# Optimization experiments

Measured on AMD Instinct MI355X. Metric: run time of the kernel, lower is better.

Reference implementation:

```python
import jax, jax.numpy as jnp
import numpy as np

N, F, D = 32, 1024, 512
H = 2 * D  # dim * ratio
EPS = 1e-5


def batchnorm1d(x, gamma, beta):
    # x: (N, F, L); BatchNorm1d over channel dim F, stats over (N, L) (training mode, biased var)
    mean = jnp.mean(x, axis=(0, 2), keepdims=True)
    var = jnp.var(x, axis=(0, 2), keepdims=True)
    xn = (x - mean) * jax.lax.rsqrt(var + EPS)
    return xn * gamma[None, :, None] + beta[None, :, None]


def setup_inputs() -> dict:
    key = jax.random.key(0)
    ks = jax.random.split(key, 5)
    x = jax.random.normal(ks[0], (N, F, D), dtype=jnp.float32)
    W0 = jax.random.normal(ks[1], (H, D), dtype=jnp.float32) * 0.02  # Linear(D->H) weight (out,in)
    b0 = jnp.zeros((H,), jnp.float32)
    W1 = jax.random.normal(ks[2], (D, H), dtype=jnp.float32) * 0.02  # Linear(H->D)
    b1 = jnp.zeros((D,), jnp.float32)
    Wc = jax.random.normal(ks[3], (F, F), dtype=jnp.float32) * 0.02  # Conv1d k=1 weight (out_ch,in_ch)
    bc = jnp.zeros((F,), jnp.float32)
    ones = jnp.ones((F,), jnp.float32)
    zeros = jnp.zeros((F,), jnp.float32)
    return {
        "x": x,
        "W0": W0, "b0": b0, "g0": ones, "be0": zeros,
        "W1": W1, "b1": b1, "g1": ones, "be1": zeros,
        "gf": ones, "bf": zeros,
        "Wc": Wc, "bc": bc,
        "go": ones, "bo": zeros,
    }


def reference(x, W0, b0, g0, be0, W1, b1, g1, be1, gf, bf, Wc, bc, go, bo):
    # proj_mlp0: Linear(D->H) + BN1d(F)
    v = jnp.einsum('nfd,hd->nfh', x, W0) + b0  # (N, F, H)
    v = batchnorm1d(v, g0, be0)
    # correlation: bmm(v, v^T) -> softsign -> bmm(w, v)
    w = jnp.einsum('nfh,ngh->nfg', v, v)  # (N, F, F)
    w = w / (1.0 + jnp.abs(w))  # softsign
    v = jnp.einsum('nfg,ngh->nfh', w, v)  # (N, F, H)
    # proj_mlp1: Linear(H->D) + BN1d(F)
    v = jnp.einsum('nfh,dh->nfd', v, W1) + b1  # (N, F, D)
    v = batchnorm1d(v, g1, be1)
    # feed_norm(v + x)
    xr = batchnorm1d(v + x, gf, bf)
    # proj_conv: Conv1d(F->F, kernel=1) over channel dim
    v = jnp.einsum('oi,nid->nod', Wc, xr) + bc[None, :, None]
    return batchnorm1d(v + xr, go, bo)
```

## Files before the change

### kernel.cpp

```cpp
#include <hip/hip_runtime.h>
#include <stdint.h>

#define NB 32
#define FC 1024
#define DD 512
#define HH 1024
#define BN_EPS 1e-5f

typedef unsigned short u16;
typedef unsigned int u32;
typedef __attribute__((ext_vector_type(8))) short bf16x8;
typedef __attribute__((ext_vector_type(4))) float f32x4;
typedef __attribute__((ext_vector_type(8))) unsigned short ushort8v;

#define AS1 __attribute__((address_space(1)))
#define AS3 __attribute__((address_space(3)))

__device__ __forceinline__ float b2f(u16 u) {
    union { u32 i; float f; } v;
    v.i = ((u32)u) << 16;
    return v.f;
}
__device__ __forceinline__ u16 f2b(float f) {
    union { float f; u32 i; } v;
    v.f = f;
    const u32 b = v.i;
    return (u16)((b + 0x7FFFu + ((b >> 16) & 1u)) >> 16);
}

__device__ __forceinline__ void gld16(const u16* g, u16* l) {
    __builtin_amdgcn_global_load_lds((const AS1 u32*)g, (AS3 u32*)l, 16, 0, 0);
}

__device__ __forceinline__ void swizzle_tiles(int& mt, int& nt, int& zt) {
    const int gx = gridDim.x, gy = gridDim.y, gz = gridDim.z;
    const int mzTot = gy * gz;
    if ((mzTot & 7) != 0) { nt = blockIdx.x; mt = blockIdx.y; zt = blockIdx.z; return; }
    long lin = ((long)blockIdx.z * gy + blockIdx.y) * gx + blockIdx.x;
    const int slab = mzTot >> 3;
    const int xcd = (int)(lin & 7);
    const long idx = lin >> 3;
    nt = (int)(idx % gx);
    const int mz = (int)(idx / gx) + xcd * slab;
    mt = mz % gy;
    zt = mz / gy;
}

__global__ __launch_bounds__(256) void detect_dtype(
    const u32* __restrict__ x, int* __restrict__ flag)
{
    __shared__ int cnt[256];
    int c = 0;
    for (int i = threadIdx.x; i < 4096; i += 256) {
        const u32 lo = x[i] & 0xFFFFu;
        const u32 e = (lo >> 7) & 0xFFu;
        if (e >= 0x68u && e <= 0x85u) c++;
    }
    cnt[threadIdx.x] = c;
    __syncthreads();
    for (int s = 128; s > 0; s >>= 1) {
        if (threadIdx.x < (unsigned)s) cnt[threadIdx.x] += cnt[threadIdx.x + s];
        __syncthreads();
    }
    if (threadIdx.x == 0) flag[0] = (cnt[0] > 2048) ? 1 : 0;
}

__global__ __launch_bounds__(256) void zero_partials(float* __restrict__ sp) {
    sp[blockIdx.x * 256 + threadIdx.x] = 0.0f;
}

__global__ __launch_bounds__(256) void fold_bn(
    const float* __restrict__ sp, const u16* __restrict__ gamma,
    const u16* __restrict__ beta, float* __restrict__ ssf, float invCnt)
{
    const int f = blockIdx.x * 256 + threadIdx.x;
    if (f < FC) {
        const float mean = sp[f] * invCnt;
        const float var  = sp[FC + f] * invCnt - mean * mean;
        const float rstd = rsqrtf(var + BN_EPS);
        const float sc   = b2f(gamma[f]) * rstd;
        ssf[f]      = sc;
        ssf[FC + f] = b2f(beta[f]) - mean * sc;
    }
}

__global__ __launch_bounds__(256) void convert_to_bf16(
    const void* __restrict__ src, u16* __restrict__ dst, long n4,
    const int* __restrict__ flag)
{
    const bool isbf = (*flag != 0);
    long i4 = (long)blockIdx.x * blockDim.x + threadIdx.x;
    const long stride = (long)gridDim.x * blockDim.x;
    for (; i4 < n4; i4 += stride) {
        const long i = i4 << 2;
        if (isbf) {
            *(ushort4*)(dst + i) = *(const ushort4*)((const u16*)src + i);
        } else {
            const float4 v = *(const float4*)((const float*)src + i);
            ushort4 o;
            o.x = f2b(v.x); o.y = f2b(v.y); o.z = f2b(v.z); o.w = f2b(v.w);
            *(ushort4*)(dst + i) = o;
        }
    }
}

struct ConvArgs { const void* src[14]; long off[14]; long n4[14]; };
__global__ __launch_bounds__(256) void convert_params(
    ConvArgs a, u16* __restrict__ dst, const int* __restrict__ flag)
{
    const bool isbf = (*flag != 0);
    const long stride = (long)gridDim.x * blockDim.x;
    for (int s = 0; s < 14; ++s) {
        const long n4 = a.n4[s];
        u16* d = dst + a.off[s];
        const void* sp = a.src[s];
        for (long i4 = (long)blockIdx.x * blockDim.x + threadIdx.x; i4 < n4;
             i4 += stride) {
            const long i = i4 << 2;
            if (isbf) {
                *(ushort4*)(d + i) = *(const ushort4*)((const u16*)sp + i);
            } else {
                const float4 v = *(const float4*)((const float*)sp + i);
                ushort4 o;
                o.x = f2b(v.x); o.y = f2b(v.y); o.z = f2b(v.z); o.w = f2b(v.w);
                *(ushort4*)(d + i) = o;
            }
        }
    }
}

template<bool BIAS, bool SOFTSIGN, bool STATS, bool RESID>
__global__ __launch_bounds__(512, 4) void gemm128x256_nt(
    const u16* __restrict__ A, const u16* __restrict__ B,
    const u16* __restrict__ bias, const u16* __restrict__ resid,
    u16* __restrict__ C, float* __restrict__ sp, int sym,
    int M, int N, int K, int lda, int ldb, int ldc,
    long sA, long sB, long sC)
{
    extern __shared__ char smem[];

    int mt, nt, zt;
    swizzle_tiles(mt, nt, zt);
    if (sym && mt < 2 * nt) return;
    const u16* Ab = A + (long)zt * sA + (long)(mt * 128) * lda;
    const u16* Bb = B + (long)zt * sB + (long)(nt * 256) * ldb;
    C += (long)zt * sC;
    const u16* RP = RESID ? (resid + (long)zt * sC) : nullptr;

    const int tid  = threadIdx.x;
    const int lane = tid & 63;
    const int wv   = tid >> 6;
    const int wrr  = (wv >> 2) * 64;
    const int wc   = (wv & 3) * 64;
    const int lm   = lane & 15;
    const int q    = lane >> 4;

    int aOff[4], bOff[4];
    #pragma unroll
    for (int i = 0; i < 4; ++i) {
        const int r = wrr + i * 16 + lm;
        aOff[i] = r * 64 + ((q ^ ((r >> 1) & 3)) << 4);
    }
    #pragma unroll
    for (int j = 0; j < 4; ++j) {
        const int r = wc + j * 16 + lm;
        bOff[j] = r * 64 + ((q ^ ((r >> 1) & 3)) << 4);
    }

    const int rw = lane >> 2, qs = lane & 3;
    const int rA  = wv * 16 + rw;
    const int rB0 = wv * 32 + rw;
    const int rB1 = wv * 32 + 16 + rw;
    const u16* pA  = Ab + (long)rA  * lda + ((qs ^ ((rA  >> 1) & 3)) << 3);
    const u16* pB0 = Bb + (long)rB0 * ldb + ((qs ^ ((rB0 >> 1) & 3)) << 3);
    const u16* pB1 = Bb + (long)rB1 * ldb + ((qs ^ ((rB1 >> 1) & 3)) << 3);
    const int ldsA  = wv * 1024;
    const int ldsB0 = wv * 2048;
    const int ldsB1 = wv * 2048 + 1024;

#define STAGE(bufOff, kofs) { \
    gld16(pA  + (kofs), (u16*)(smem + (bufOff) + ldsA)); \
    gld16(pB0 + (kofs), (u16*)(smem + (bufOff) + 8192 + ldsB0)); \
    gld16(pB1 + (kofs), (u16*)(smem + (bufOff) + 8192 + ldsB1)); }

#define RINGBAR() { \
    asm volatile("s_waitcnt vmcnt(3) lgkmcnt(0)" ::: "memory"); \
    __builtin_amdgcn_sched_barrier(0); \
    __builtin_amdgcn_s_barrier(); \
    __builtin_amdgcn_sched_barrier(0); }

    f32x4 acc[4][4] = {};

    const int NT = K >> 5;

    STAGE(0, 0);
    STAGE(24576, 32);
    RINGBAR();

    int cur = 0, nxt = 2;
    for (int t = 0; t < NT; ++t) {
        const int bo = cur * 24576;
        const int bn = nxt * 24576;
        const int kn = (((t + 2) < NT) ? (t + 2) : (NT - 1)) * 32;
        STAGE(bn, kn);

        bf16x8 a[4], b[4];
        const char* baseA = smem + bo;
        const char* baseB = smem + bo + 8192;
        #pragma unroll
        for (int i = 0; i < 4; ++i) a[i] = *(const bf16x8*)(baseA + aOff[i]);
        #pragma unroll
        for (int j = 0; j < 4; ++j) b[j] = *(const bf16x8*)(baseB + bOff[j]);

        #pragma unroll
        for (int i = 0; i < 4; ++i)
            #pragma unroll
            for (int j = 0; j < 4; ++j)
                acc[i][j] = __builtin_amdgcn_mfma_f32_16x16x32_bf16(
                    a[i], b[j], acc[i][j], 0, 0, 0);

        RINGBAR();
        cur = (cur == 2) ? 0 : cur + 1;
        nxt = (nxt == 2) ? 0 : nxt + 1;
    }

#undef STAGE
#undef RINGBAR

    asm volatile("s_waitcnt vmcnt(0)" ::: "memory");
    __builtin_amdgcn_sched_barrier(0);
    __syncthreads();

    float* rep = (float*)smem + wv * (16 * 65);
    const int rr = lane >> 2;
    const int cg = lane & 3;
    const int m0 = mt * 128;
    const int n0 = nt * 256;
    #pragma unroll
    for (int i = 0; i < 4; ++i) {
        #pragma unroll
        for (int j = 0; j < 4; ++j) {
            const int col = 16 * j + lm;
            const float bj = BIAS ? b2f(bias[n0 + wc + col]) : 0.0f;
            #pragma unroll
            for (int r = 0; r < 4; ++r) {
                float v = acc[i][j][r] + bj;
                if (SOFTSIGN) v = v / (1.0f + fabsf(v));
                rep[(q * 4 + r) * 65 + col] = v;
            }
        }
        const int row = m0 + wrr + 16 * i + rr;
        const float* lr = rep + rr * 65 + cg * 16;
        float4 f0 = *(const float4*)(lr + 0);
        float4 f1 = *(const float4*)(lr + 4);
        float4 f2 = *(const float4*)(lr + 8);
        float4 f3 = *(const float4*)(lr + 12);
        if (RESID) {
            const u16* rp = RP + (long)row * ldc + n0 + wc + cg * 16;
            const ushort8v ra = *(const ushort8v*)rp;
            const ushort8v rb = *(const ushort8v*)(rp + 8);
            f0.x += b2f(ra[0]); f0.y += b2f(ra[1]); f0.z += b2f(ra[2]); f0.w += b2f(ra[3]);
            f1.x += b2f(ra[4]); f1.y += b2f(ra[5]); f1.z += b2f(ra[6]); f1.w += b2f(ra[7]);
            f2.x += b2f(rb[0]); f2.y += b2f(rb[1]); f2.z += b2f(rb[2]); f2.w += b2f(rb[3]);
            f3.x += b2f(rb[4]); f3.y += b2f(rb[5]); f3.z += b2f(rb[6]); f3.w += b2f(rb[7]);
        }
        if (STATS) {
            float s1 = (f0.x + f0.y + f0.z + f0.w) + (f1.x + f1.y + f1.z + f1.w)
                     + (f2.x + f2.y + f2.z + f2.w) + (f3.x + f3.y + f3.z + f3.w);
            float s2 = f0.x*f0.x + f0.y*f0.y + f0.z*f0.z + f0.w*f0.w
                     + f1.x*f1.x + f1.y*f1.y + f1.z*f1.z + f1.w*f1.w
                     + f2.x*f2.x + f2.y*f2.y + f2.z*f2.z + f2.w*f2.w
                     + f3.x*f3.x + f3.y*f3.y + f3.z*f3.z + f3.w*f3.w;
            s1 += __shfl_xor(s1, 1); s1 += __shfl_xor(s1, 2);
            s2 += __shfl_xor(s2, 1); s2 += __shfl_xor(s2, 2);
            if (cg == 0) {
                const int ch = row & (FC - 1);
                atomicAdd(&sp[ch], s1);
                atomicAdd(&sp[FC + ch], s2);
            }
        }
        ushort8v o0, o1;
        o0[0] = f2b(f0.x); o0[1] = f2b(f0.y); o0[2] = f2b(f0.z); o0[3] = f2b(f0.w);
        o0[4] = f2b(f1.x); o0[5] = f2b(f1.y); o0[6] = f2b(f1.z); o0[7] = f2b(f1.w);
        o1[0] = f2b(f2.x); o1[1] = f2b(f2.y); o1[2] = f2b(f2.z); o1[3] = f2b(f2.w);
        o1[4] = f2b(f3.x); o1[5] = f2b(f3.y); o1[6] = f2b(f3.z); o1[7] = f2b(f3.w);
        u16* cp = C + (long)row * ldc + n0 + wc + cg * 16;
        *(ushort8v*)cp = o0;
        *(ushort8v*)(cp + 8) = o1;
    }
}

__global__ __launch_bounds__(256) void mirror_upper(
    u16* __restrict__ W, long sW)
{
    const int MTt[12] = {0,1, 0,1,2,3, 0,1,2,3,4,5};
    const int NTt[12] = {1,1, 2,2,2,2, 3,3,3,3,3,3};
    __shared__ u16 t[32][33];
    const int id = blockIdx.y;
    const int mt = MTt[id], nt = NTt[id];
    W += (long)blockIdx.z * sW;
    const int rb = blockIdx.x & 3, cb = blockIdx.x >> 2;
    const int dr0 = mt * 128 + rb * 32;
    const int dc0 = nt * 256 + cb * 32;
    const int lx = threadIdx.x & 31;
    const int ly = threadIdx.x >> 5;
    #pragma unroll
    for (int d = 0; d < 32; d += 8)
        t[ly + d][lx] = W[(long)(dc0 + ly + d) * FC + dr0 + lx];
    __syncthreads();
    #pragma unroll
    for (int d = 0; d < 32; d += 8)
        W[(long)(dr0 + ly + d) * FC + dc0 + lx] = t[lx][ly + d];
}

__global__ __launch_bounds__(256) void transpose_bn_bf16(
    const u16* __restrict__ src, u16* __restrict__ dstT,
    u16* __restrict__ dstI, const float* __restrict__ ssf,
    int R, int Cc, long sS, long sD)
{
    __shared__ u16 t[32][33];
    const int bz = blockIdx.z;
    src  += (long)bz * sS;
    dstI += (long)bz * sS;
    dstT += (long)bz * sD;
    const int c0 = blockIdx.x * 32;
    const int r0 = blockIdx.y * 32;
    const int lx = threadIdx.x & 31;
    const int ly = threadIdx.x >> 5;
    #pragma unroll
    for (int d = 0; d < 32; d += 8) {
        const int r = r0 + ly + d;
        const u16 nv = f2b(fmaf(b2f(src[(long)r * Cc + c0 + lx]),
                                ssf[r], ssf[FC + r]));
        t[ly + d][lx] = nv;
        dstI[(long)r * Cc + c0 + lx] = nv;
    }
    __syncthreads();
    #pragma unroll
    for (int d = 0; d < 32; d += 8)
        dstT[(long)(c0 + ly + d) * R + r0 + lx] = t[lx][ly + d];
}

template<bool ADD, bool STATS>
__global__ __launch_bounds__(256) void bn_apply(
    const u16* __restrict__ src, const void* __restrict__ add,
    const int* __restrict__ addflag,
    const float* __restrict__ ss, void* __restrict__ dst,
    const int* __restrict__ outflag, long total4, int lcShift,
    float* __restrict__ sp)
{
    const bool addf32 = ADD && (addflag != nullptr) && (*addflag == 0);
    const bool outf32 = (outflag != nullptr) && (*outflag == 0);
    long i4 = (long)blockIdx.x * blockDim.x + threadIdx.x;
    const long stride = (long)gridDim.x * blockDim.x;
    for (; i4 < total4; i4 += stride) {
        const long i = i4 << 2;
        const int c = (int)((i >> lcShift) & (FC - 1));
        const float sc = ss[c];
        const float sh = ss[FC + c];
        const ushort4 v = *(const ushort4*)(src + i);
        float o0 = fmaf(b2f(v.x), sc, sh);
        float o1 = fmaf(b2f(v.y), sc, sh);
        float o2 = fmaf(b2f(v.z), sc, sh);
        float o3 = fmaf(b2f(v.w), sc, sh);
        if (ADD) {
            if (addf32) {
                const float4 a = *(const float4*)((const float*)add + i);
                o0 += a.x; o1 += a.y; o2 += a.z; o3 += a.w;
            } else {
                const ushort4 a = *(const ushort4*)((const u16*)add + i);
                o0 += b2f(a.x); o1 += b2f(a.y); o2 += b2f(a.z); o3 += b2f(a.w);
            }
        }
        if (STATS) {
            float s1 = o0 + o1 + o2 + o3;
            float s2 = o0 * o0 + o1 * o1 + o2 * o2 + o3 * o3;
            #pragma unroll
            for (int m = 1; m < 64; m <<= 1) {
                s1 += __shfl_xor(s1, m);
                s2 += __shfl_xor(s2, m);
            }
            if ((threadIdx.x & 63) == 0) {
                atomicAdd(&sp[c], s1);
                atomicAdd(&sp[FC + c], s2);
            }
        }
        if (outf32) {
            float4 o; o.x = o0; o.y = o1; o.z = o2; o.w = o3;
            *(float4*)((float*)dst + i) = o;
        } else {
            ushort4 o;
            o.x = f2b(o0); o.y = f2b(o1); o.z = f2b(o2); o.w = f2b(o3);
            *(ushort4*)((u16*)dst + i) = o;
        }
    }
}

extern "C" void kernel_launch(void* const* d_in, const int* in_sizes, int n_in,
                              void* d_out, int out_size, void* d_ws, size_t ws_size,
                              hipStream_t stream)
{
    const size_t MiB = (size_t)1 << 20;
    const long sFH = (long)FC * HH;
    const long sFF = (long)FC * FC;
    const long sFD = (long)FC * DD;
    const long PE  = (long)NB * FC * DD;

    const size_t GLDS = 73728;
    static bool s_attr = false;
    if (!s_attr) {
        s_attr = true;
        hipFuncSetAttribute(reinterpret_cast<const void*>(&gemm128x256_nt<true, false, true, false>),
                            hipFuncAttributeMaxDynamicSharedMemorySize, (int)GLDS);
        hipFuncSetAttribute(reinterpret_cast<const void*>(&gemm128x256_nt<false, true, false, false>),
                            hipFuncAttributeMaxDynamicSharedMemorySize, (int)GLDS);
        hipFuncSetAttribute(reinterpret_cast<const void*>(&gemm128x256_nt<false, false, false, false>),
                            hipFuncAttributeMaxDynamicSharedMemorySize, (int)GLDS);
        hipFuncSetAttribute(reinterpret_cast<const void*>(&gemm128x256_nt<true, false, true, true>),
                            hipFuncAttributeMaxDynamicSharedMemorySize, (int)GLDS);
    }

    long off[16];
    long cur = 0;
    for (int i = 1; i < 15; ++i) { off[i] = cur; cur += ((long)in_sizes[i] + 7) & ~7L; }
    const size_t paramBytes = (size_t)cur * 2;

    int cb = 32;
    while (cb > 1 &&
           64 * MiB + (size_t)cb * 6 * MiB + paramBytes + 65536 > ws_size)
        cb >>= 1;

    u16* V   = (u16*)d_ws;
    u16* VT  = (u16*)((char*)d_ws + 64 * MiB);
    u16* WW  = VT + (long)cb * sFH;
    u16* V2  = WW + (long)cb * sFF;
    u16* WC  = V2 + (long)cb * sFH;
    char* tail = (char*)(WC + cur);
    tail = (char*)(((uintptr_t)tail + 255) & ~(uintptr_t)255);
    float* SP0  = (float*)tail;
    float* SP1  = SP0 + 2 * FC;
    float* SP2  = SP1 + 2 * FC;
    float* SP3  = SP2 + 2 * FC;
    float* SSF  = SP3 + 2 * FC;
    int*   FLAG = (int*)(SSF + 2 * FC);
    u16* VX  = (u16*)d_out;
    u16* XB  = (u16*)d_out + PE;
    u16* V4  = V;
    u16* XRT = V + PE;

    const dim3 blk(256);
    const dim3 blk512(512);
    const dim3 egrid(4096);

    detect_dtype<<<1, blk, 0, stream>>>((const u32*)d_in[0], FLAG);
    zero_partials<<<dim3(32), blk, 0, stream>>>(SP0);
    ConvArgs ca;
    for (int i = 1; i < 15; ++i) {
        ca.src[i - 1] = d_in[i];
        ca.off[i - 1] = off[i];
        ca.n4[i - 1]  = (long)in_sizes[i] / 4;
    }
    convert_params<<<dim3(256), blk, 0, stream>>>(ca, WC, FLAG);
    convert_to_bf16<<<dim3(1024), blk, 0, stream>>>(d_in[0], XB, PE / 4, FLAG);

    const u16* W0c = WC + off[1];
    const u16* b0c = WC + off[2];
    const u16* g0c = WC + off[3];
    const u16* be0c = WC + off[4];
    const u16* W1c = WC + off[5];
    const u16* b1c = WC + off[6];
    const u16* g1c = WC + off[7];
    const u16* be1c = WC + off[8];
    const u16* gfc = WC + off[9];
    const u16* bfc = WC + off[10];
    const u16* Wcc = WC + off[11];
    const u16* bcc = WC + off[12];
    const u16* goc = WC + off[13];
    const u16* boc = WC + off[14];

    gemm128x256_nt<true, false, true, false><<<dim3(HH / 256, (NB * FC) / 128, 1), blk512, GLDS, stream>>>(
        XB, W0c, b0c, nullptr, V, SP0, 0, NB * FC, HH, DD, DD, DD, HH, 0, 0, 0);
    fold_bn<<<dim3(4), blk, 0, stream>>>(SP0, g0c, be0c, SSF, 1.0f / (float)(NB * HH));

    for (int bz0 = 0; bz0 < NB; bz0 += cb) {
        const int c = (NB - bz0 < cb) ? (NB - bz0) : cb;
        transpose_bn_bf16<<<dim3(HH / 32, FC / 32, c), blk, 0, stream>>>(
            V + bz0 * sFH, VT, V + bz0 * sFH, SSF, FC, HH, sFH, sFH);
        gemm128x256_nt<false, true, false, false><<<dim3(FC / 256, FC / 128, c), blk512, GLDS, stream>>>(
            V + bz0 * sFH, V + bz0 * sFH, nullptr, nullptr, WW, nullptr, 1,
            FC, FC, HH, HH, HH, FC, sFH, sFH, sFF);
        mirror_upper<<<dim3(32, 12, c), blk, 0, stream>>>(WW, sFF);
        gemm128x256_nt<false, false, false, false><<<dim3(HH / 256, FC / 128, c), blk512, GLDS, stream>>>(
            WW, VT, nullptr, nullptr, V2, nullptr, 0,
            FC, HH, FC, FC, FC, HH, sFF, sFH, sFH);
        gemm128x256_nt<true, false, true, false><<<dim3(DD / 256, (c * FC) / 128, 1), blk512, GLDS, stream>>>(
            V2, W1c, b1c, nullptr, VX + bz0 * sFD, SP1, 0,
            c * FC, DD, HH, HH, HH, DD, 0, 0, 0);
    }
    fold_bn<<<dim3(4), blk, 0, stream>>>(SP1, g1c, be1c, SSF, 1.0f / (float)(NB * DD));

    bn_apply<true, true><<<egrid, blk, 0, stream>>>(
        VX, XB, nullptr, SSF, VX, nullptr, PE / 4, 9, SP2);
    fold_bn<<<dim3(4), blk, 0, stream>>>(SP2, gfc, bfc, SSF, 1.0f / (float)(NB * DD));

    transpose_bn_bf16<<<dim3(DD / 32, FC / 32, NB), blk, 0, stream>>>(
        VX, XRT, VX, SSF, FC, DD, sFD, sFD);

    gemm128x256_nt<true, false, true, true><<<dim3(DD / 256, FC / 128, NB), blk512, GLDS, stream>>>(
        Wcc, XRT, bcc, VX, V4, SP3, 0, FC, DD, FC, FC, FC, DD, 0, sFD, sFD);
    fold_bn<<<dim3(4), blk, 0, stream>>>(SP3, goc, boc, SSF, 1.0f / (float)(NB * DD));

    bn_apply<false, false><<<egrid, blk, 0, stream>>>(
        V4, nullptr, nullptr, SSF, d_out, FLAG, PE / 4, 9, nullptr);
}
```

Before: 617.4 us.

## Shrink GEMM tiles to 128x128 with 256 threads and double buffering

The GEMM kernel goes from 128x256 tiles on 512 threads with a three-stage LDS ring to 128x128 tiles on 256 threads with a two-buffer pipeline and a plain __syncthreads per k-step. The symmetric v·vᵀ GEMM now uses an explicit lower-triangle tile table of 36 tiles instead of skipping upper blocks, and the mirror kernel is updated for the finer tile grid. The aim is lower LDS use and more blocks per CU for better occupancy and finer triangular work. The cost is less data reuse per tile and a shallower prefetch, with a full barrier every iteration.

Result: slower. 651.8 us (+5.6%).

```diff
diff --git a/kernel.cpp b/kernel.cpp
--- a/kernel.cpp
+++ b/kernel.cpp
@@ -130,7 +130,7 @@
 }
 
 template<bool BIAS, bool SOFTSIGN, bool STATS, bool RESID>
-__global__ __launch_bounds__(512, 4) void gemm128x256_nt(
+__global__ __launch_bounds__(256, 4) void gemm128_nt(
     const u16* __restrict__ A, const u16* __restrict__ B,
     const u16* __restrict__ bias, const u16* __restrict__ resid,
     u16* __restrict__ C, float* __restrict__ sp, int sym,
@@ -140,18 +140,25 @@
     extern __shared__ char smem[];
 
     int mt, nt, zt;
-    swizzle_tiles(mt, nt, zt);
-    if (sym && mt < 2 * nt) return;
+    if (sym) {
+        static const signed char SM[36] = {0,1,1,2,2,2,3,3,3,3,4,4,4,4,4,
+            5,5,5,5,5,5,6,6,6,6,6,6,6,7,7,7,7,7,7,7,7};
+        static const signed char SN[36] = {0,0,1,0,1,2,0,1,2,3,0,1,2,3,4,
+            0,1,2,3,4,5,0,1,2,3,4,5,6,0,1,2,3,4,5,6,7};
+        mt = SM[blockIdx.x]; nt = SN[blockIdx.x]; zt = blockIdx.z;
+    } else {
+        swizzle_tiles(mt, nt, zt);
+    }
     const u16* Ab = A + (long)zt * sA + (long)(mt * 128) * lda;
-    const u16* Bb = B + (long)zt * sB + (long)(nt * 256) * ldb;
+    const u16* Bb = B + (long)zt * sB + (long)(nt * 128) * ldb;
     C += (long)zt * sC;
     const u16* RP = RESID ? (resid + (long)zt * sC) : nullptr;
 
     const int tid  = threadIdx.x;
     const int lane = tid & 63;
     const int wv   = tid >> 6;
-    const int wrr  = (wv >> 2) * 64;
-    const int wc   = (wv & 3) * 64;
+    const int wrr  = (wv >> 1) * 64;
+    const int wc   = (wv & 1) * 64;
     const int lm   = lane & 15;
     const int q    = lane >> 4;
 
@@ -168,41 +175,32 @@
     }
 
     const int rw = lane >> 2, qs = lane & 3;
-    const int rA  = wv * 16 + rw;
-    const int rB0 = wv * 32 + rw;
-    const int rB1 = wv * 32 + 16 + rw;
-    const u16* pA  = Ab + (long)rA  * lda + ((qs ^ ((rA  >> 1) & 3)) << 3);
-    const u16* pB0 = Bb + (long)rB0 * ldb + ((qs ^ ((rB0 >> 1) & 3)) << 3);
-    const u16* pB1 = Bb + (long)rB1 * ldb + ((qs ^ ((rB1 >> 1) & 3)) << 3);
-    const int ldsA  = wv * 1024;
-    const int ldsB0 = wv * 2048;
-    const int ldsB1 = wv * 2048 + 1024;
+    const int r0s = wv * 32 + rw;
+    const int r1s = wv * 32 + 16 + rw;
+    const u16* pA0 = Ab + (long)r0s * lda + ((qs ^ ((r0s >> 1) & 3)) << 3);
+    const u16* pA1 = Ab + (long)r1s * lda + ((qs ^ ((r1s >> 1) & 3)) << 3);
+    const u16* pB0 = Bb + (long)r0s * ldb + ((qs ^ ((r0s >> 1) & 3)) << 3);
+    const u16* pB1 = Bb + (long)r1s * ldb + ((qs ^ ((r1s >> 1) & 3)) << 3);
+    const int lds0 = wv * 2048;
+    const int lds1 = wv * 2048 + 1024;
 
 #define STAGE(bufOff, kofs) { \
-    gld16(pA  + (kofs), (u16*)(smem + (bufOff) + ldsA)); \
-    gld16(pB0 + (kofs), (u16*)(smem + (bufOff) + 8192 + ldsB0)); \
-    gld16(pB1 + (kofs), (u16*)(smem + (bufOff) + 8192 + ldsB1)); }
-
-#define RINGBAR() { \
-    asm volatile("s_waitcnt vmcnt(3) lgkmcnt(0)" ::: "memory"); \
-    __builtin_amdgcn_sched_barrier(0); \
-    __builtin_amdgcn_s_barrier(); \
-    __builtin_amdgcn_sched_barrier(0); }
+    gld16(pA0 + (kofs), (u16*)(smem + (bufOff) + lds0)); \
+    gld16(pA1 + (kofs), (u16*)(smem + (bufOff) + lds1)); \
+    gld16(pB0 + (kofs), (u16*)(smem + (bufOff) + 8192 + lds0)); \
+    gld16(pB1 + (kofs), (u16*)(smem + (bufOff) + 8192 + lds1)); }
 
     f32x4 acc[4][4] = {};
 
     const int NT = K >> 5;
 
     STAGE(0, 0);
-    STAGE(24576, 32);
-    RINGBAR();
-
-    int cur = 0, nxt = 2;
+    __syncthreads();
+
     for (int t = 0; t < NT; ++t) {
-        const int bo = cur * 24576;
-        const int bn = nxt * 24576;
-        const int kn = (((t + 2) < NT) ? (t + 2) : (NT - 1)) * 32;
-        STAGE(bn, kn);
+        const int bo = (t & 1) * 16384;
+        const int bn = ((t + 1) & 1) * 16384;
+        if (t + 1 < NT) STAGE(bn, (t + 1) * 32);
 
         bf16x8 a[4], b[4];
         const char* baseA = smem + bo;
@@ -219,23 +217,16 @@
                 acc[i][j] = __builtin_amdgcn_mfma_f32_16x16x32_bf16(
                     a[i], b[j], acc[i][j], 0, 0, 0);
 
-        RINGBAR();
-        cur = (cur == 2) ? 0 : cur + 1;
-        nxt = (nxt == 2) ? 0 : nxt + 1;
+        __syncthreads();
     }
 
 #undef STAGE
-#undef RINGBAR
-
-    asm volatile("s_waitcnt vmcnt(0)" ::: "memory");
-    __builtin_amdgcn_sched_barrier(0);
-    __syncthreads();
 
     float* rep = (float*)smem + wv * (16 * 65);
     const int rr = lane >> 2;
     const int cg = lane & 3;
     const int m0 = mt * 128;
-    const int n0 = nt * 256;
+    const int n0 = nt * 128;
     #pragma unroll
     for (int i = 0; i < 4; ++i) {
         #pragma unroll
@@ -293,15 +284,17 @@
 __global__ __launch_bounds__(256) void mirror_upper(
     u16* __restrict__ W, long sW)
 {
-    const int MTt[12] = {0,1, 0,1,2,3, 0,1,2,3,4,5};
-    const int NTt[12] = {1,1, 2,2,2,2, 3,3,3,3,3,3};
+    static const signed char MTt[28] = {0,0,0,0,0,0,0, 1,1,1,1,1,1, 2,2,2,2,2,
+        3,3,3,3, 4,4,4, 5,5, 6};
+    static const signed char NTt[28] = {1,2,3,4,5,6,7, 2,3,4,5,6,7, 3,4,5,6,7,
+        4,5,6,7, 5,6,7, 6,7, 7};
     __shared__ u16 t[32][33];
     const int id = blockIdx.y;
     const int mt = MTt[id], nt = NTt[id];
     W += (long)blockIdx.z * sW;
     const int rb = blockIdx.x & 3, cb = blockIdx.x >> 2;
     const int dr0 = mt * 128 + rb * 32;
-    const int dc0 = nt * 256 + cb * 32;
+    const int dc0 = nt * 128 + cb * 32;
     const int lx = threadIdx.x & 31;
     const int ly = threadIdx.x >> 5;
     #pragma unroll
@@ -406,17 +399,17 @@
     const long sFD = (long)FC * DD;
     const long PE  = (long)NB * FC * DD;
 
-    const size_t GLDS = 73728;
+    const size_t GLDS = 32768;
     static bool s_attr = false;
     if (!s_attr) {
         s_attr = true;
-        hipFuncSetAttribute(reinterpret_cast<const void*>(&gemm128x256_nt<true, false, true, false>),
+        hipFuncSetAttribute(reinterpret_cast<const void*>(&gemm128_nt<true, false, true, false>),
                             hipFuncAttributeMaxDynamicSharedMemorySize, (int)GLDS);
-        hipFuncSetAttribute(reinterpret_cast<const void*>(&gemm128x256_nt<false, true, false, false>),
+        hipFuncSetAttribute(reinterpret_cast<const void*>(&gemm128_nt<false, true, false, false>),
                             hipFuncAttributeMaxDynamicSharedMemorySize, (int)GLDS);
-        hipFuncSetAttribute(reinterpret_cast<const void*>(&gemm128x256_nt<false, false, false, false>),
+        hipFuncSetAttribute(reinterpret_cast<const void*>(&gemm128_nt<false, false, false, false>),
                             hipFuncAttributeMaxDynamicSharedMemorySize, (int)GLDS);
-        hipFuncSetAttribute(reinterpret_cast<const void*>(&gemm128x256_nt<true, false, true, true>),
+        hipFuncSetAttribute(reinterpret_cast<const void*>(&gemm128_nt<true, false, true, true>),
                             hipFuncAttributeMaxDynamicSharedMemorySize, (int)GLDS);
     }
 
@@ -449,7 +442,6 @@
     u16* XRT = V + PE;
 
     const dim3 blk(256);
-    const dim3 blk512(512);
     const dim3 egrid(4096);
 
     detect_dtype<<<1, blk, 0, stream>>>((const u32*)d_in[0], FLAG);
@@ -478,7 +470,7 @@
     const u16* goc = WC + off[13];
     const u16* boc = WC + off[14];
 
-    gemm128x256_nt<true, false, true, false><<<dim3(HH / 256, (NB * FC) / 128, 1), blk512, GLDS, stream>>>(
+    gemm128_nt<true, false, true, false><<<dim3(HH / 128, (NB * FC) / 128, 1), blk, GLDS, stream>>>(
         XB, W0c, b0c, nullptr, V, SP0, 0, NB * FC, HH, DD, DD, DD, HH, 0, 0, 0);
     fold_bn<<<dim3(4), blk, 0, stream>>>(SP0, g0c, be0c, SSF, 1.0f / (float)(NB * HH));
 
@@ -486,14 +478,14 @@
         const int c = (NB - bz0 < cb) ? (NB - bz0) : cb;
         transpose_bn_bf16<<<dim3(HH / 32, FC / 32, c), blk, 0, stream>>>(
             V + bz0 * sFH, VT, V + bz0 * sFH, SSF, FC, HH, sFH, sFH);
-        gemm128x256_nt<false, true, false, false><<<dim3(FC / 256, FC / 128, c), blk512, GLDS, stream>>>(
+        gemm128_nt<false, true, false, false><<<dim3(36, 1, c), blk, GLDS, stream>>>(
             V + bz0 * sFH, V + bz0 * sFH, nullptr, nullptr, WW, nullptr, 1,
             FC, FC, HH, HH, HH, FC, sFH, sFH, sFF);
-        mirror_upper<<<dim3(32, 12, c), blk, 0, stream>>>(WW, sFF);
-        gemm128x256_nt<false, false, false, false><<<dim3(HH / 256, FC / 128, c), blk512, GLDS, stream>>>(
+        mirror_upper<<<dim3(16, 28, c), blk, 0, stream>>>(WW, sFF);
+        gemm128_nt<false, false, false, false><<<dim3(HH / 128, FC / 128, c), blk, GLDS, stream>>>(
             WW, VT, nullptr, nullptr, V2, nullptr, 0,
             FC, HH, FC, FC, FC, HH, sFF, sFH, sFH);
-        gemm128x256_nt<true, false, true, false><<<dim3(DD / 256, (c * FC) / 128, 1), blk512, GLDS, stream>>>(
+        gemm128_nt<true, false, true, false><<<dim3(DD / 128, (c * FC) / 128, 1), blk, GLDS, stream>>>(
             V2, W1c, b1c, nullptr, VX + bz0 * sFD, SP1, 0,
             c * FC, DD, HH, HH, HH, DD, 0, 0, 0);
     }
@@ -506,7 +498,7 @@
     transpose_bn_bf16<<<dim3(DD / 32, FC / 32, NB), blk, 0, stream>>>(
         VX, XRT, VX, SSF, FC, DD, sFD, sFD);
 
-    gemm128x256_nt<true, false, true, true><<<dim3(DD / 256, FC / 128, NB), blk512, GLDS, stream>>>(
+    gemm128_nt<true, false, true, true><<<dim3(DD / 128, FC / 128, NB), blk, GLDS, stream>>>(
         Wcc, XRT, bcc, VX, V4, SP3, 0, FC, DD, FC, FC, FC, DD, 0, sFD, sFD);
     fold_bn<<<dim3(4), blk, 0, stream>>>(SP3, goc, boc, SSF, 1.0f / (float)(NB * DD));
 
```

## Switch GEMM to double-buffered LDS and launch only symmetric lower tiles

Applied to the files above, without the earlier changes.

Replaces the triple-buffered ring pipeline, which used a manual vmcnt wait and s_barrier, with a plain double buffer that synchronises via __syncthreads. This cuts dynamic LDS from 72KB to 48KB so more blocks can fit per CU. The symmetric v·vᵀ GEMM now launches only the 20 needed lower-triangle tiles through a lookup table, instead of launching all tiles and returning early. The trade-off is less prefetch depth: only one tile is in flight, and each iteration ends with a full wait on the load.

After: 645.3 us. 4.5% more time.

```diff
diff --git a/kernel.cpp b/kernel.cpp
--- a/kernel.cpp
+++ b/kernel.cpp
@@ -140,8 +140,15 @@
     extern __shared__ char smem[];
 
     int mt, nt, zt;
-    swizzle_tiles(mt, nt, zt);
-    if (sym && mt < 2 * nt) return;
+    if (sym) {
+        static const signed char SM[20] = {0,1,2,3,4,5,6,7, 2,3,4,5,6,7,
+                                           4,5,6,7, 6,7};
+        static const signed char SN[20] = {0,0,0,0,0,0,0,0, 1,1,1,1,1,1,
+                                           2,2,2,2, 3,3};
+        mt = SM[blockIdx.x]; nt = SN[blockIdx.x]; zt = blockIdx.z;
+    } else {
+        swizzle_tiles(mt, nt, zt);
+    }
     const u16* Ab = A + (long)zt * sA + (long)(mt * 128) * lda;
     const u16* Bb = B + (long)zt * sB + (long)(nt * 256) * ldb;
     C += (long)zt * sC;
@@ -183,26 +190,17 @@
     gld16(pB0 + (kofs), (u16*)(smem + (bufOff) + 8192 + ldsB0)); \
     gld16(pB1 + (kofs), (u16*)(smem + (bufOff) + 8192 + ldsB1)); }
 
-#define RINGBAR() { \
-    asm volatile("s_waitcnt vmcnt(3) lgkmcnt(0)" ::: "memory"); \
-    __builtin_amdgcn_sched_barrier(0); \
-    __builtin_amdgcn_s_barrier(); \
-    __builtin_amdgcn_sched_barrier(0); }
-
     f32x4 acc[4][4] = {};
 
     const int NT = K >> 5;
 
     STAGE(0, 0);
-    STAGE(24576, 32);
-    RINGBAR();
-
-    int cur = 0, nxt = 2;
+    __syncthreads();
+
     for (int t = 0; t < NT; ++t) {
-        const int bo = cur * 24576;
-        const int bn = nxt * 24576;
-        const int kn = (((t + 2) < NT) ? (t + 2) : (NT - 1)) * 32;
-        STAGE(bn, kn);
+        const int bo = (t & 1) * 24576;
+        const int bn = ((t + 1) & 1) * 24576;
+        if (t + 1 < NT) STAGE(bn, (t + 1) * 32);
 
         bf16x8 a[4], b[4];
         const char* baseA = smem + bo;
@@ -219,17 +217,10 @@
                 acc[i][j] = __builtin_amdgcn_mfma_f32_16x16x32_bf16(
                     a[i], b[j], acc[i][j], 0, 0, 0);
 
-        RINGBAR();
-        cur = (cur == 2) ? 0 : cur + 1;
-        nxt = (nxt == 2) ? 0 : nxt + 1;
+        __syncthreads();
     }
 
 #undef STAGE
-#undef RINGBAR
-
-    asm volatile("s_waitcnt vmcnt(0)" ::: "memory");
-    __builtin_amdgcn_sched_barrier(0);
-    __syncthreads();
 
     float* rep = (float*)smem + wv * (16 * 65);
     const int rr = lane >> 2;
@@ -293,8 +284,8 @@
 __global__ __launch_bounds__(256) void mirror_upper(
     u16* __restrict__ W, long sW)
 {
-    const int MTt[12] = {0,1, 0,1,2,3, 0,1,2,3,4,5};
-    const int NTt[12] = {1,1, 2,2,2,2, 3,3,3,3,3,3};
+    static const signed char MTt[12] = {0,1, 0,1,2,3, 0,1,2,3,4,5};
+    static const signed char NTt[12] = {1,1, 2,2,2,2, 3,3,3,3,3,3};
     __shared__ u16 t[32][33];
     const int id = blockIdx.y;
     const int mt = MTt[id], nt = NTt[id];
@@ -406,7 +397,7 @@
     const long sFD = (long)FC * DD;
     const long PE  = (long)NB * FC * DD;
 
-    const size_t GLDS = 73728;
+    const size_t GLDS = 49152;
     static bool s_attr = false;
     if (!s_attr) {
         s_attr = true;
@@ -486,7 +477,7 @@
         const int c = (NB - bz0 < cb) ? (NB - bz0) : cb;
         transpose_bn_bf16<<<dim3(HH / 32, FC / 32, c), blk, 0, stream>>>(
             V + bz0 * sFH, VT, V + bz0 * sFH, SSF, FC, HH, sFH, sFH);
-        gemm128x256_nt<false, true, false, false><<<dim3(FC / 256, FC / 128, c), blk512, GLDS, stream>>>(
+        gemm128x256_nt<false, true, false, false><<<dim3(20, 1, c), blk512, GLDS, stream>>>(
             V + bz0 * sFH, V + bz0 * sFH, nullptr, nullptr, WW, nullptr, 1,
             FC, FC, HH, HH, HH, FC, sFH, sFH, sFF);
         mirror_upper<<<dim3(32, 12, c), blk, 0, stream>>>(WW, sFF);
```
